# Performance work log

Hardware: AMD Instinct MI355X
Metric: run time of the kernel (lower is better)

The kernel has to match this reference:

```python
import jax, jax.numpy as jnp
import numpy as np

T = 1.0
N_NEG = 50
NUM_CLASSES = 500  # smoothing denominator K from CrossEntropyLabelSmooth (faithful quirk)
EPS = 0.1

B, C, D = 2048, 65536, 256


def setup_inputs() -> dict:
    key = jax.random.key(0)
    k1, k2, k3 = jax.random.split(key, 3)
    f = jax.random.normal(k1, (B, D), dtype=jnp.float32)
    centers = jax.random.normal(k2, (C, D), dtype=jnp.float32)
    label = jax.random.randint(k3, (B,), 0, C, dtype=jnp.int64)
    return {"f": f, "centers": centers, "label": label}


def reference(f, centers, label):
    b = f.shape[0]
    rows = jnp.arange(b)
    mat = f @ centers.T                              # [B, C] similarity scores
    pos = mat[rows, label][:, None]                  # [B, 1] positive score
    # mask the positive column so top-k picks only negatives
    masked = mat.at[rows, label].set(-jnp.inf)
    neg, _ = jax.lax.top_k(masked, N_NEG)            # [B, N_neg]
    preds = jnp.concatenate([pos, neg], axis=1) / T  # [B, 1 + N_neg]
    log_probs = jax.nn.log_softmax(preds, axis=1)
    # label-smoothed one-hot with target class 0 (the positive)
    onehot = jnp.zeros_like(log_probs).at[:, 0].set(1.0)
    targets = (1.0 - EPS) * onehot + EPS / NUM_CLASSES
    loss = (-targets * log_probs).mean(0).sum()
    return loss
```

## Files before the change

### kernel.cpp

```cpp
#include <hip/hip_runtime.h>
#include <hip/hip_fp16.h>

#define B_ROWS 2048
#define C_COLS 65536
#define D_DIM  256
#define N_NEG  50
#define NTILES (C_COLS / 128)

typedef __attribute__((ext_vector_type(8))) short short8;
typedef __attribute__((ext_vector_type(4))) float floatx4;
typedef __fp16 f16x2 __attribute__((ext_vector_type(2)));

__device__ __forceinline__ ushort f2bf(float f) {
  unsigned u = __float_as_uint(f);
  unsigned r = (u + 0x7FFFu + ((u >> 16) & 1u)) >> 16;
  return (ushort)r;
}

__device__ __forceinline__ uint hmax2(uint a, uint b) {
  union { uint u; f16x2 h; } x, y, r;
  x.u = a; y.u = b;
  r.h = __builtin_elementwise_max(x.h, y.h);
  return r.u;
}

__global__ void cvt_swz(const float* __restrict__ in, ushort* __restrict__ out, int n8) {
  int i = blockIdx.x * blockDim.x + threadIdx.x;
  if (i >= n8) return;
  int row = i >> 5;
  int ka  = i & 31;
  int ktile = ka >> 3, kb = ka & 7;
  const float4* src = (const float4*)(in + (size_t)i * 8);
  float4 a = src[0], b = src[1];
  ushort4 o0, o1;
  o0.x = f2bf(a.x); o0.y = f2bf(a.y); o0.z = f2bf(a.z); o0.w = f2bf(a.w);
  o1.x = f2bf(b.x); o1.y = f2bf(b.y); o1.z = f2bf(b.z); o1.w = f2bf(b.w);
  ushort* dst = out + (size_t)row * D_DIM + ktile * 64 + ((kb ^ (row & 7)) << 3);
  ((ushort4*)dst)[0] = o0;
  ((ushort4*)dst)[1] = o1;
}

__device__ __forceinline__ void async16(const void* g, void* l) {
  __builtin_amdgcn_global_load_lds((const __attribute__((address_space(1))) void*)g,
                                   (__attribute__((address_space(3))) void*)l,
                                   16, 0, 0);
}

template <bool PREB>
__global__ void gemm_reduce(const ushort* __restrict__ fb,
                            const ushort* __restrict__ cb,
                            const float* __restrict__ cen,
                            const int* __restrict__ label,
                            ushort* __restrict__ cand) {
  __shared__ __align__(16) ushort Cs[128 * 64];
  __shared__ __align__(16) ushort Fs[128 * 64];
  __shared__ __align__(16) ushort gm[128][8];
  __shared__ int labLDS[128];

  const int tid = threadIdx.x, wave = tid >> 6, lane = tid & 63;
  const int l = lane & 15, q = lane >> 4;

  const int lin = blockIdx.y * 16 + blockIdx.x;
  const int lg  = (lin & 7) * 1024 + (lin >> 3);
  const int m0 = (lg & 15) << 7;
  const int bxTile = lg >> 4;
  const int n0 = bxTile << 7;
  if (tid < 128) labLDS[tid] = label[m0 + tid];

  floatx4 acc[4][4] = {};
  const int wn = (wave >> 1) * 64, wm = (wave & 1) * 64;

  for (int kt = 0; kt < D_DIM / 64; ++kt) {
#pragma unroll
    for (int r = 0; r < 4; ++r) {
      int idx = r * 2048 + wave * 512 + lane * 8;
      int row = idx >> 6, kk = idx & 63;
      async16(fb + (size_t)(m0 + row) * D_DIM + kt * 64 + kk, Fs + r * 2048 + wave * 512);
      if (PREB)
        async16(cb + (size_t)(n0 + row) * D_DIM + kt * 64 + kk, Cs + r * 2048 + wave * 512);
    }
    if (!PREB) {
      float4 ra[4], rb[4];
#pragma unroll
      for (int g = 0; g < 4; ++g) {
        int e = (tid + g * 256) * 8;
        const float* gp = cen + (size_t)(n0 + (e >> 6)) * D_DIM + kt * 64 + (e & 63);
        ra[g] = *(const float4*)gp;
        rb[g] = *(const float4*)(gp + 4);
      }
#pragma unroll
      for (int g = 0; g < 4; ++g) {
        int e = (tid + g * 256) * 8;
        int row = e >> 6, kblk = (e >> 3) & 7;
        uint4 o;
        o.x = (uint)f2bf(ra[g].x) | ((uint)f2bf(ra[g].y) << 16);
        o.y = (uint)f2bf(ra[g].z) | ((uint)f2bf(ra[g].w) << 16);
        o.z = (uint)f2bf(rb[g].x) | ((uint)f2bf(rb[g].y) << 16);
        o.w = (uint)f2bf(rb[g].z) | ((uint)f2bf(rb[g].w) << 16);
        *(uint4*)(Cs + (row << 6) + ((kblk ^ (row & 7)) << 3)) = o;
      }
    }
    __syncthreads();

#pragma unroll
    for (int ks = 0; ks < 2; ++ks) {
      short8 a[4], b[4];
#pragma unroll
      for (int i = 0; i < 4; ++i) {
        int swz = ((4 * ks + q) ^ (l & 7)) << 3;
        a[i] = *(const short8*)(Cs + ((wn + i * 16 + l) << 6) + swz);
        b[i] = *(const short8*)(Fs + ((wm + i * 16 + l) << 6) + swz);
      }
#pragma unroll
      for (int i = 0; i < 4; ++i)
#pragma unroll
        for (int j = 0; j < 4; ++j)
          acc[i][j] = __builtin_amdgcn_mfma_f32_16x16x32_bf16(a[i], b[j], acc[i][j], 0, 0, 0);
    }
    __syncthreads();
  }

  int lj[4];
#pragma unroll
  for (int j = 0; j < 4; ++j) lj[j] = labLDS[wm + j * 16 + l] - n0 - wn;
  bool hit = false;
#pragma unroll
  for (int j = 0; j < 4; ++j) hit = hit || ((unsigned)lj[j] < 64u);
  if (__any(hit)) {
#pragma unroll
    for (int j = 0; j < 4; ++j) {
      int relq = lj[j] - q * 4;
#pragma unroll
      for (int i = 0; i < 4; ++i) {
        int rel = relq - i * 16;
#pragma unroll
        for (int r = 0; r < 4; ++r)
          if (rel == r) acc[i][j][r] = -INFINITY;
      }
    }
  }
#pragma unroll
  for (int j = 0; j < 4; ++j) {
    float mx[4];
#pragma unroll
    for (int i = 0; i < 4; ++i)
      mx[i] = fmaxf(fmaxf(acc[i][j][0], acc[i][j][1]),
                    fmaxf(acc[i][j][2], acc[i][j][3]));
    union { f16x2 h; uint u; } c0, c1;
    c0.h = __builtin_amdgcn_cvt_pkrtz(mx[0], mx[1]);
    c1.h = __builtin_amdgcn_cvt_pkrtz(mx[2], mx[3]);
    uint u01 = c0.u, u23 = c1.u;
    u01 = hmax2(u01, __shfl_xor(u01, 16));
    u01 = hmax2(u01, __shfl_xor(u01, 32));
    u23 = hmax2(u23, __shfl_xor(u23, 16));
    u23 = hmax2(u23, __shfl_xor(u23, 32));
    if (q == 0) {
      uint2 w; w.x = u01; w.y = u23;
      *(uint2*)&gm[wm + j * 16 + l][wn >> 4] = w;
    }
  }
  __syncthreads();
  if (tid < 128) {
    uint4 w = *(const uint4*)&gm[tid][0];
    *(uint4*)(cand + ((size_t)bxTile * B_ROWS + (m0 + tid)) * 8) = w;
  }
}

__device__ __forceinline__ float dec_key(int k) {
  if (k < 0x0400) return -INFINITY;
  ushort h = (k >= 0x8000) ? (ushort)(k ^ 0x8000) : (ushort)(~k & 0xFFFF);
  __half_raw hr; hr.x = h;
  return __half2float((__half)hr);
}

__global__ __launch_bounds__(512) void final_select(const ushort* __restrict__ cand,
                                                    const float* __restrict__ f,
                                                    const float* __restrict__ cen,
                                                    const int* __restrict__ label,
                                                    float* __restrict__ rowloss) {
  __shared__ __align__(16) uint4 ST[NTILES][8];
  const int tid = threadIdx.x;
  const int lane = tid & 63, w = tid >> 6;
  const int row0 = blockIdx.x * 8;

  const uint4* p = (const uint4*)cand;
#pragma unroll
  for (int k = 0; k < 8; ++k) {
    int j = k * 512 + tid;
    int tile = j >> 3, rr = j & 7;
    ST[tile][rr ^ (tile & 7)] = p[(size_t)tile * B_ROWS + row0 + rr];
  }
  __syncthreads();

  const int row = row0 + w;
  const int lab = label[row];

  float v[64];
#pragma unroll
  for (int c = 0; c < 8; ++c) {
    int tile = c * 64 + lane;
    uint4 u = ST[tile][w ^ (tile & 7)];
    union { uint u; f16x2 h; } cv;
    cv.u = u.x; v[c * 8 + 0] = (float)cv.h.x; v[c * 8 + 1] = (float)cv.h.y;
    cv.u = u.y; v[c * 8 + 2] = (float)cv.h.x; v[c * 8 + 3] = (float)cv.h.y;
    cv.u = u.z; v[c * 8 + 4] = (float)cv.h.x; v[c * 8 + 5] = (float)cv.h.y;
    cv.u = u.w; v[c * 8 + 6] = (float)cv.h.x; v[c * 8 + 7] = (float)cv.h.y;
  }

  float4 fv = *(const float4*)(f   + (size_t)row * D_DIM + lane * 4);
  float4 cv4 = *(const float4*)(cen + (size_t)lab * D_DIM + lane * 4);
  float pv = fv.x * cv4.x + fv.y * cv4.y + fv.z * cv4.z + fv.w * cv4.w;

  float m = v[0];
#pragma unroll
  for (int k = 1; k < 64; ++k) m = fmaxf(m, v[k]);
#pragma unroll
  for (int o = 32; o > 0; o >>= 1) {
    m = fmaxf(m, __shfl_xor(m, o));
    pv += __shfl_xor(pv, o);
  }
  const float pos = pv;

  __half hm = __float2half(m);
  int hb = (int)(*(ushort*)&hm);
  int km = (m >= 0.f) ? (0x8000 | hb) : (~hb & 0xFFFF);
  int lo = km - 2048, hi = km;
  if (lo < 0x0400) lo = 0x0400;
  for (int it = 0; it < 12; ++it) {
    int mid = (lo + hi) >> 1;
    float tau = dec_key(mid);
    int c = 0;
#pragma unroll
    for (int k = 0; k < 64; ++k) c += (v[k] > tau) ? 1 : 0;
#pragma unroll
    for (int o = 32; o > 0; o >>= 1) c += __shfl_xor(c, o);
    if (c <= 49) hi = mid; else lo = mid + 1;
  }

  const float tau = dec_key(hi);
  float sum = 0.f, se = 0.f; int c = 0;
#pragma unroll
  for (int k = 0; k < 64; ++k) {
    if (v[k] > tau) { ++c; sum += v[k]; se += expf(v[k] - m); }
  }
#pragma unroll
  for (int o = 32; o > 0; o >>= 1) {
    sum += __shfl_xor(sum, o);
    se  += __shfl_xor(se, o);
    c   += __shfl_xor(c, o);
  }
  if (lane == 0) {
    float nfill = (float)(N_NEG - c);
    float S = sum + nfill * tau;
    float E = se + nfill * expf(tau - m);
    float M = fmaxf(m, pos);
    float seAll = E * expf(m - M) + expf(pos - M);
    float lse = M + logf(seAll);
    rowloss[row] = 0.9102f * lse - 0.9002f * pos - 2.0e-4f * S;
  }
}

__global__ void sum_loss(const float* __restrict__ rowloss, float* __restrict__ out) {
  __shared__ float red[4];
  const int tid = threadIdx.x;
  float s = 0.f;
  for (int i = tid; i < B_ROWS; i += 256) s += rowloss[i];
#pragma unroll
  for (int o = 32; o > 0; o >>= 1) s += __shfl_down(s, o);
  if ((tid & 63) == 0) red[tid >> 6] = s;
  __syncthreads();
  if (tid == 0) out[0] = (red[0] + red[1] + red[2] + red[3]) * (1.0f / B_ROWS);
}

extern "C" void kernel_launch(void* const* d_in, const int* in_sizes, int n_in,
                              void* d_out, int out_size, void* d_ws, size_t ws_size,
                              hipStream_t stream) {
  const float* f   = (const float*)d_in[0];
  const float* cen = (const float*)d_in[1];
  const int*   label = (const int*)d_in[2];
  float* out = (float*)d_out;

  char* ws = (char*)d_ws;
  ushort* cand    = (ushort*)ws;
  ushort* fb      = (ushort*)(ws + 16777216);
  float*  rowloss = (float*)(ws + 17825792);
  ushort* cb      = (ushort*)(ws + 17833984);
  const bool pre = ws_size >= (17833984ull + 33554432ull);

  cvt_swz<<<256, 256, 0, stream>>>(f, fb, (B_ROWS * D_DIM) / 8);

  dim3 grid(B_ROWS / 128, NTILES);
  if (pre) {
    cvt_swz<<<8192, 256, 0, stream>>>(cen, cb, (C_COLS * D_DIM) / 8);
    gemm_reduce<true><<<grid, 256, 0, stream>>>(fb, cb, nullptr, label, cand);
  } else {
    gemm_reduce<false><<<grid, 256, 0, stream>>>(fb, nullptr, cen, label, cand);
  }

  final_select<<<B_ROWS / 8, 512, 0, stream>>>(cand, f, cen, label, rowloss);
  sum_loss<<<1, 256, 0, stream>>>(rowloss, out);
}
```

Before: 190.1 us.

## Make centers tile resident in LDS and stream all f rows per block

The GEMM is restructured so each block loads one 128-row centers tile once, converts it from fp32 to bf16 in-kernel, and keeps the full K=256 in LDS. It then loops over all 16 row-tiles of f, double-buffering the bf16 f tiles with async global-to-LDS loads. This removes the separate centers conversion pass and the 32MB bf16 centers buffer, and reads each centers row from global memory only once. The cost is a 512-block grid at 512 threads with 96KB of LDS per block, so fewer blocks fit per CU, and candidate maxima are now written straight to global memory without staging in LDS.

Measured after the change: 220.3 us. 15.9% more time.

```diff
diff --git a/kernel.cpp b/kernel.cpp
--- a/kernel.cpp
+++ b/kernel.cpp
@@ -46,123 +46,120 @@
                                    16, 0, 0);
 }
 
-template <bool PREB>
-__global__ void gemm_reduce(const ushort* __restrict__ fb,
-                            const ushort* __restrict__ cb,
-                            const float* __restrict__ cen,
-                            const int* __restrict__ label,
-                            ushort* __restrict__ cand) {
-  __shared__ __align__(16) ushort Cs[128 * 64];
-  __shared__ __align__(16) ushort Fs[128 * 64];
-  __shared__ __align__(16) ushort gm[128][8];
-  __shared__ int labLDS[128];
+__global__ __launch_bounds__(512, 2) void gemm_reduce(const ushort* __restrict__ fb,
+                                                      const float* __restrict__ cen,
+                                                      const int* __restrict__ label,
+                                                      ushort* __restrict__ cand) {
+  __shared__ __align__(16) ushort Cs[4 * 8192];
+  __shared__ __align__(16) ushort Fs[2 * 8192];
 
   const int tid = threadIdx.x, wave = tid >> 6, lane = tid & 63;
   const int l = lane & 15, q = lane >> 4;
 
-  const int lin = blockIdx.y * 16 + blockIdx.x;
-  const int lg  = (lin & 7) * 1024 + (lin >> 3);
-  const int m0 = (lg & 15) << 7;
-  const int bxTile = lg >> 4;
-  const int n0 = bxTile << 7;
-  if (tid < 128) labLDS[tid] = label[m0 + tid];
-
-  floatx4 acc[4][4] = {};
-  const int wn = (wave >> 1) * 64, wm = (wave & 1) * 64;
-
-  for (int kt = 0; kt < D_DIM / 64; ++kt) {
-#pragma unroll
-    for (int r = 0; r < 4; ++r) {
-      int idx = r * 2048 + wave * 512 + lane * 8;
-      int row = idx >> 6, kk = idx & 63;
-      async16(fb + (size_t)(m0 + row) * D_DIM + kt * 64 + kk, Fs + r * 2048 + wave * 512);
-      if (PREB)
-        async16(cb + (size_t)(n0 + row) * D_DIM + kt * 64 + kk, Cs + r * 2048 + wave * 512);
+  const int b = blockIdx.x;
+  const int tile = (b & 7) * 64 + (b >> 3);
+  const int n0 = tile << 7;
+
+#pragma unroll
+  for (int g = 0; g < 8; ++g) {
+    int e = (g * 512 + tid) * 8;
+    int row = e >> 8, k = e & 255;
+    const float* gp = cen + (size_t)(n0 + row) * D_DIM + k;
+    float4 fa = *(const float4*)gp;
+    float4 fbv = *(const float4*)(gp + 4);
+    int kt = k >> 6, kblk = (k >> 3) & 7;
+    uint4 o;
+    o.x = (uint)f2bf(fa.x)  | ((uint)f2bf(fa.y)  << 16);
+    o.y = (uint)f2bf(fa.z)  | ((uint)f2bf(fa.w)  << 16);
+    o.z = (uint)f2bf(fbv.x) | ((uint)f2bf(fbv.y) << 16);
+    o.w = (uint)f2bf(fbv.z) | ((uint)f2bf(fbv.w) << 16);
+    *(uint4*)(Cs + kt * 8192 + (row << 6) + ((kblk ^ (row & 7)) << 3)) = o;
+  }
+
+#pragma unroll
+  for (int r = 0; r < 2; ++r) {
+    int idx = r * 4096 + wave * 512 + lane * 8;
+    int row = idx >> 6, kk = idx & 63;
+    async16(fb + (size_t)row * D_DIM + kk, Fs + r * 4096 + wave * 512);
+  }
+  __syncthreads();
+
+  const int wn = (wave & 1) * 64, wm = (wave >> 1) * 32;
+
+  for (int s = 0; s < 16; ++s) {
+    floatx4 acc[4][2] = {};
+    const int m0 = s << 7;
+#pragma unroll
+    for (int kt = 0; kt < 4; ++kt) {
+      const int step = s * 4 + kt;
+      if (step + 1 < 64) {
+        const int ns = (step + 1) >> 2, nkt = (step + 1) & 3, nb = (step + 1) & 1;
+#pragma unroll
+        for (int r = 0; r < 2; ++r) {
+          int idx = r * 4096 + wave * 512 + lane * 8;
+          int row = idx >> 6, kk = idx & 63;
+          async16(fb + (size_t)((ns << 7) + row) * D_DIM + nkt * 64 + kk,
+                  Fs + nb * 8192 + r * 4096 + wave * 512);
+        }
+      }
+      const ushort* Cb = Cs + kt * 8192;
+      const ushort* Fb = Fs + (step & 1) * 8192;
+#pragma unroll
+      for (int ks = 0; ks < 2; ++ks) {
+        short8 a[4], bb[2];
+        int swz = ((4 * ks + q) ^ (l & 7)) << 3;
+#pragma unroll
+        for (int i = 0; i < 4; ++i)
+          a[i] = *(const short8*)(Cb + ((wn + i * 16 + l) << 6) + swz);
+#pragma unroll
+        for (int j = 0; j < 2; ++j)
+          bb[j] = *(const short8*)(Fb + ((wm + j * 16 + l) << 6) + swz);
+#pragma unroll
+        for (int i = 0; i < 4; ++i)
+#pragma unroll
+          for (int j = 0; j < 2; ++j)
+            acc[i][j] = __builtin_amdgcn_mfma_f32_16x16x32_bf16(a[i], bb[j], acc[i][j], 0, 0, 0);
+      }
+      __syncthreads();
     }
-    if (!PREB) {
-      float4 ra[4], rb[4];
-#pragma unroll
-      for (int g = 0; g < 4; ++g) {
-        int e = (tid + g * 256) * 8;
-        const float* gp = cen + (size_t)(n0 + (e >> 6)) * D_DIM + kt * 64 + (e & 63);
-        ra[g] = *(const float4*)gp;
-        rb[g] = *(const float4*)(gp + 4);
-      }
-#pragma unroll
-      for (int g = 0; g < 4; ++g) {
-        int e = (tid + g * 256) * 8;
-        int row = e >> 6, kblk = (e >> 3) & 7;
-        uint4 o;
-        o.x = (uint)f2bf(ra[g].x) | ((uint)f2bf(ra[g].y) << 16);
-        o.y = (uint)f2bf(ra[g].z) | ((uint)f2bf(ra[g].w) << 16);
-        o.z = (uint)f2bf(rb[g].x) | ((uint)f2bf(rb[g].y) << 16);
-        o.w = (uint)f2bf(rb[g].z) | ((uint)f2bf(rb[g].w) << 16);
-        *(uint4*)(Cs + (row << 6) + ((kblk ^ (row & 7)) << 3)) = o;
+
+    int lj[2];
+#pragma unroll
+    for (int j = 0; j < 2; ++j) lj[j] = label[m0 + wm + j * 16 + l] - n0 - wn;
+    bool hit = ((unsigned)lj[0] < 64u) || ((unsigned)lj[1] < 64u);
+    if (__any(hit)) {
+#pragma unroll
+      for (int j = 0; j < 2; ++j) {
+        int relq = lj[j] - q * 4;
+#pragma unroll
+        for (int i = 0; i < 4; ++i) {
+          int rel = relq - i * 16;
+#pragma unroll
+          for (int r = 0; r < 4; ++r)
+            if (rel == r) acc[i][j][r] = -INFINITY;
+        }
       }
     }
-    __syncthreads();
-
-#pragma unroll
-    for (int ks = 0; ks < 2; ++ks) {
-      short8 a[4], b[4];
-#pragma unroll
-      for (int i = 0; i < 4; ++i) {
-        int swz = ((4 * ks + q) ^ (l & 7)) << 3;
-        a[i] = *(const short8*)(Cs + ((wn + i * 16 + l) << 6) + swz);
-        b[i] = *(const short8*)(Fs + ((wm + i * 16 + l) << 6) + swz);
-      }
+#pragma unroll
+    for (int j = 0; j < 2; ++j) {
+      float mx[4];
 #pragma unroll
       for (int i = 0; i < 4; ++i)
-#pragma unroll
-        for (int j = 0; j < 4; ++j)
-          acc[i][j] = __builtin_amdgcn_mfma_f32_16x16x32_bf16(a[i], b[j], acc[i][j], 0, 0, 0);
+        mx[i] = fmaxf(fmaxf(acc[i][j][0], acc[i][j][1]),
+                      fmaxf(acc[i][j][2], acc[i][j][3]));
+      union { f16x2 h; uint u; } c0, c1;
+      c0.h = __builtin_amdgcn_cvt_pkrtz(mx[0], mx[1]);
+      c1.h = __builtin_amdgcn_cvt_pkrtz(mx[2], mx[3]);
+      uint u01 = c0.u, u23 = c1.u;
+      u01 = hmax2(u01, __shfl_xor(u01, 16));
+      u01 = hmax2(u01, __shfl_xor(u01, 32));
+      u23 = hmax2(u23, __shfl_xor(u23, 16));
+      u23 = hmax2(u23, __shfl_xor(u23, 32));
+      if (q == 0) {
+        uint2 w; w.x = u01; w.y = u23;
+        *(uint2*)(cand + ((size_t)tile * B_ROWS + m0 + wm + j * 16 + l) * 8 + (wn >> 4)) = w;
+      }
     }
-    __syncthreads();
-  }
-
-  int lj[4];
-#pragma unroll
-  for (int j = 0; j < 4; ++j) lj[j] = labLDS[wm + j * 16 + l] - n0 - wn;
-  bool hit = false;
-#pragma unroll
-  for (int j = 0; j < 4; ++j) hit = hit || ((unsigned)lj[j] < 64u);
-  if (__any(hit)) {
-#pragma unroll
-    for (int j = 0; j < 4; ++j) {
-      int relq = lj[j] - q * 4;
-#pragma unroll
-      for (int i = 0; i < 4; ++i) {
-        int rel = relq - i * 16;
-#pragma unroll
-        for (int r = 0; r < 4; ++r)
-          if (rel == r) acc[i][j][r] = -INFINITY;
-      }
-    }
-  }
-#pragma unroll
-  for (int j = 0; j < 4; ++j) {
-    float mx[4];
-#pragma unroll
-    for (int i = 0; i < 4; ++i)
-      mx[i] = fmaxf(fmaxf(acc[i][j][0], acc[i][j][1]),
-                    fmaxf(acc[i][j][2], acc[i][j][3]));
-    union { f16x2 h; uint u; } c0, c1;
-    c0.h = __builtin_amdgcn_cvt_pkrtz(mx[0], mx[1]);
-    c1.h = __builtin_amdgcn_cvt_pkrtz(mx[2], mx[3]);
-    uint u01 = c0.u, u23 = c1.u;
-    u01 = hmax2(u01, __shfl_xor(u01, 16));
-    u01 = hmax2(u01, __shfl_xor(u01, 32));
-    u23 = hmax2(u23, __shfl_xor(u23, 16));
-    u23 = hmax2(u23, __shfl_xor(u23, 32));
-    if (q == 0) {
-      uint2 w; w.x = u01; w.y = u23;
-      *(uint2*)&gm[wm + j * 16 + l][wn >> 4] = w;
-    }
-  }
-  __syncthreads();
-  if (tid < 128) {
-    uint4 w = *(const uint4*)&gm[tid][0];
-    *(uint4*)(cand + ((size_t)bxTile * B_ROWS + (m0 + tid)) * 8) = w;
   }
 }
 
@@ -284,18 +281,10 @@
   ushort* cand    = (ushort*)ws;
   ushort* fb      = (ushort*)(ws + 16777216);
   float*  rowloss = (float*)(ws + 17825792);
-  ushort* cb      = (ushort*)(ws + 17833984);
-  const bool pre = ws_size >= (17833984ull + 33554432ull);
 
   cvt_swz<<<256, 256, 0, stream>>>(f, fb, (B_ROWS * D_DIM) / 8);
 
-  dim3 grid(B_ROWS / 128, NTILES);
-  if (pre) {
-    cvt_swz<<<8192, 256, 0, stream>>>(cen, cb, (C_COLS * D_DIM) / 8);
-    gemm_reduce<true><<<grid, 256, 0, stream>>>(fb, cb, nullptr, label, cand);
-  } else {
-    gemm_reduce<false><<<grid, 256, 0, stream>>>(fb, nullptr, cen, label, cand);
-  }
+  gemm_reduce<<<NTILES, 512, 0, stream>>>(fb, cen, label, cand);
 
   final_select<<<B_ROWS / 8, 512, 0, stream>>>(cand, f, cen, label, rowloss);
   sum_loss<<<1, 256, 0, stream>>>(rowloss, out);
```
